# Optimization experiments

Measured on AMD Instinct MI355X. Metric: run time of the kernel, lower is better.

The kernel has to match this reference:

```python
import jax, jax.numpy as jnp
import numpy as np

EMB_DIM = 1024
ATT_DIM = 1024

def setup_inputs() -> dict:
    key = jax.random.key(0)
    ks = jax.random.split(key, 7)
    B, S = 8, 2048
    x_h = jax.random.normal(ks[0], (B, S, EMB_DIM), dtype=jnp.float32)
    # Linear params (stored as [in, out] for x @ W + b)
    sq = 1.0 / np.sqrt(EMB_DIM)
    Wq = jax.random.uniform(ks[1], (EMB_DIM, ATT_DIM), jnp.float32, -sq, sq)
    bq = jax.random.uniform(ks[2], (ATT_DIM,), jnp.float32, -sq, sq)
    Wk = jax.random.uniform(ks[3], (EMB_DIM, ATT_DIM), jnp.float32, -sq, sq)
    bk = jax.random.uniform(ks[4], (ATT_DIM,), jnp.float32, -sq, sq)
    Wv = jax.random.uniform(ks[5], (EMB_DIM, EMB_DIM), jnp.float32, -sq, sq)
    bv = jax.random.uniform(ks[6], (EMB_DIM,), jnp.float32, -sq, sq)
    return {"x_h": x_h, "Wq": Wq, "bq": bq, "Wk": Wk, "bk": bk, "Wv": Wv, "bv": bv}

def reference(x_h, Wq, bq, Wk, bk, Wv, bv):
    q = x_h @ Wq + bq               # [B,S,att_dim]
    k = x_h @ Wk + bk               # [B,S,att_dim]
    v = x_h @ Wv + bv               # [B,S,emb_dim]
    scale = 1.0 / jnp.sqrt(jnp.asarray(k.shape[-1], q.dtype))
    scores = jnp.einsum('bqd,bkd->bqk', q, k) * scale   # [B,S,S]
    # NOTE: original softmaxes over dim=1 (the QUERY axis), not the key axis.
    attn = jax.nn.softmax(scores, axis=1)
    return jnp.einsum('bqk,bkd->bqd', attn, v)
```

## Files before the change

kernel.cpp:

```cpp
#include <hip/hip_runtime.h>
#include <math.h>

typedef __bf16 bf16x8 __attribute__((ext_vector_type(8)));
typedef float f32x4 __attribute__((ext_vector_type(4)));
typedef unsigned short ushort8 __attribute__((ext_vector_type(8)));
typedef unsigned short u16;

#define DEVINL __device__ __forceinline__

DEVINL u16 f2bf(float f) {
    union { float f; unsigned u; } a; a.f = f;
    unsigned u = a.u;
    return (u16)((u + 0x7FFFu + ((u >> 16) & 1u)) >> 16);
}
DEVINL float bf2f(u16 h) { return __uint_as_float(((unsigned)h) << 16); }

DEVINL void gload_lds16(const void* g, void* l) {
    __builtin_amdgcn_global_load_lds(
        (__attribute__((address_space(1))) void*)(g),
        (__attribute__((address_space(3))) void*)(l),
        16, 0, 0);
}

template<int EPI>
__global__ __launch_bounds__(512, 2)
void gemm256(const u16* __restrict__ A, int lda, long sAz,
             const u16* __restrict__ B, int ldb, long sBz,
             void* __restrict__ Cv, int ldc, long sCz,
             const float* __restrict__ bias, float scale, int K)
{
    __shared__ u16 lds[65536];
    const int tid = threadIdx.x;
    const long bz = blockIdx.z;
    const u16* Ab = A + bz * sAz;
    const u16* Bb = B + bz * sBz;
    const int row0 = blockIdx.x * 256, col0 = blockIdx.y * 256;

    const int sr = tid >> 2;
    const int csw = ((tid & 3) * 16) ^ (((sr >> 1) & 3) << 4);
    const u16* Ag = Ab + (long)(row0 + sr) * lda + (csw >> 1);
    const u16* Bg = Bb + (long)(col0 + sr) * ldb + (csw >> 1);
    const int dst0 = tid * 8;

    const int lane = tid & 63, wid = tid >> 6;
    const int wm = wid >> 2, wn = wid & 3;
    const int lane_r = lane & 15;
    const int rdcol = (((lane >> 4) * 16) ^ (((lane_r >> 1) & 3) << 4)) >> 1;
    const int arow0 = wm * 128 + lane_r;
    const int brow0 = wn * 64 + lane_r;

    const int NT = K >> 6;
    f32x4 acc[8][4] = {};
    bf16x8 af[4], bfrag[4];

    auto issueA = [&](int t1, int s, int buf) {
        const u16* g = Ag + (long)t1 * 64 + s * 32;
        u16* d = &lds[(buf * 2 + s) * 8192 + dst0];
        gload_lds16(g, d);
        gload_lds16(g + (long)128 * lda, d + 4096);
    };
    auto issueB = [&](int t1, int s, int buf) {
        const u16* g = Bg + (long)t1 * 64 + s * 32;
        u16* d = &lds[32768 + (buf * 2 + s) * 8192 + dst0];
        gload_lds16(g, d);
        gload_lds16(g + (long)128 * ldb, d + 4096);
    };

#define READ_A(s, h)                                                        \
    _Pragma("unroll")                                                       \
    for (int m = 0; m < 4; ++m)                                             \
        af[m] = *(const bf16x8*)&lds[(buf * 2 + (s)) * 8192 +               \
                     (arow0 + (h) * 64 + m * 16) * 32 + rdcol];

#define READ_B(s)                                                           \
    _Pragma("unroll")                                                       \
    for (int n = 0; n < 4; ++n)                                             \
        bfrag[n] = *(const bf16x8*)&lds[32768 + (buf * 2 + (s)) * 8192 +    \
                     (brow0 + n * 16) * 32 + rdcol];

#define MFMA16(h)                                                           \
    __builtin_amdgcn_s_setprio(1);                                          \
    _Pragma("unroll")                                                       \
    for (int m = 0; m < 4; ++m)                                             \
        _Pragma("unroll")                                                   \
        for (int n = 0; n < 4; ++n)                                         \
            acc[(h) * 4 + m][n] = __builtin_amdgcn_mfma_f32_16x16x32_bf16(  \
                af[m], bfrag[n], acc[(h) * 4 + m][n], 0, 0, 0);             \
    __builtin_amdgcn_s_setprio(0);

    issueA(0, 0, 0); issueB(0, 0, 0); issueA(0, 1, 0); issueB(0, 1, 0);
    asm volatile("s_waitcnt vmcnt(4)" ::: "memory");
    __builtin_amdgcn_s_barrier();

    for (int t = 0; t < NT - 1; ++t) {
        const int buf = t & 1, nbuf = buf ^ 1;
        READ_A(0, 0); READ_B(0);
        issueA(t + 1, 0, nbuf);
        __builtin_amdgcn_s_barrier();
        MFMA16(0);
        __builtin_amdgcn_s_barrier();
        READ_A(0, 1);
        issueB(t + 1, 0, nbuf);
        asm volatile("s_waitcnt vmcnt(4)" ::: "memory");
        __builtin_amdgcn_s_barrier();
        MFMA16(1);
        __builtin_amdgcn_s_barrier();
        READ_A(1, 0); READ_B(1);
        issueA(t + 1, 1, nbuf);
        __builtin_amdgcn_s_barrier();
        MFMA16(0);
        __builtin_amdgcn_s_barrier();
        READ_A(1, 1);
        issueB(t + 1, 1, nbuf);
        asm volatile("s_waitcnt vmcnt(4)" ::: "memory");
        __builtin_amdgcn_s_barrier();
        MFMA16(1);
        __builtin_amdgcn_s_barrier();
    }
    {
        const int buf = (NT - 1) & 1;
        READ_A(0, 0); READ_B(0);
        __builtin_amdgcn_s_barrier();
        MFMA16(0);
        __builtin_amdgcn_s_barrier();
        READ_A(0, 1);
        asm volatile("s_waitcnt vmcnt(0)" ::: "memory");
        __builtin_amdgcn_s_barrier();
        MFMA16(1);
        __builtin_amdgcn_s_barrier();
        READ_A(1, 0); READ_B(1);
        __builtin_amdgcn_s_barrier();
        MFMA16(0);
        __builtin_amdgcn_s_barrier();
        READ_A(1, 1);
        __builtin_amdgcn_s_barrier();
        MFMA16(1);
    }
#undef READ_A
#undef READ_B
#undef MFMA16

    const int crow = (lane >> 4) * 4, ccol = lane & 15;
#pragma unroll
    for (int mf = 0; mf < 8; ++mf)
#pragma unroll
        for (int nf = 0; nf < 4; ++nf) {
            const int gc = col0 + wn * 64 + nf * 16 + ccol;
#pragma unroll
            for (int r = 0; r < 4; ++r) {
                const int gr = row0 + wm * 128 + mf * 16 + crow + r;
                const float v = acc[mf][nf][r];
                if constexpr (EPI == 0) {
                    ((u16*)Cv)[bz * sCz + (long)gr * ldc + gc] = f2bf(v + bias[gc]);
                } else if constexpr (EPI == 1) {
                    ((u16*)Cv)[bz * sCz + (long)gr * ldc + gc] = f2bf(__expf(v * scale));
                } else {
                    ((float*)Cv)[bz * sCz + (long)gr * ldc + gc] = v;
                }
            }
        }
}

__global__ void cast_x_k(const float* __restrict__ x, u16* __restrict__ o)
{
    const int i = blockIdx.x * 256 + threadIdx.x;
    const float4* xv = (const float4*)x;
    const float4 a = xv[(long)i * 2], b = xv[(long)i * 2 + 1];
    ushort8 r;
    r[0] = f2bf(a.x); r[1] = f2bf(a.y); r[2] = f2bf(a.z); r[3] = f2bf(a.w);
    r[4] = f2bf(b.x); r[5] = f2bf(b.y); r[6] = f2bf(b.z); r[7] = f2bf(b.w);
    *(ushort8*)(o + (long)i * 8) = r;
}

__global__ void wt_k(const float* __restrict__ Wq, const float* __restrict__ Wk,
                     const float* __restrict__ Wv, u16* __restrict__ Wt)
{
    __shared__ float t[32][33];
    const int z = blockIdx.z;
    const float* W = (z == 0) ? Wq : ((z == 1) ? Wk : Wv);
    const int k0 = blockIdx.x * 32, n0 = blockIdx.y * 32;
    const int tx = threadIdx.x, ty = threadIdx.y;
#pragma unroll
    for (int j = 0; j < 32; j += 8)
        t[ty + j][tx] = W[(long)(k0 + ty + j) * 1024 + n0 + tx];
    __syncthreads();
#pragma unroll
    for (int j = 0; j < 32; j += 8)
        Wt[((long)z * 1024 + n0 + ty + j) * 1024 + k0 + tx] = f2bf(t[tx][ty + j]);
}

__global__ void bias_k(const float* __restrict__ bq, const float* __restrict__ bk,
                       const float* __restrict__ bv, float* __restrict__ bcat)
{
    const int i = blockIdx.x * 256 + threadIdx.x;
    bcat[i] = (i < 1024) ? bq[i] : ((i < 2048) ? bk[i - 1024] : bv[i - 2048]);
}

__global__ void colsum_k(const u16* __restrict__ E, float* __restrict__ part)
{
    const int b = blockIdx.z, qc = blockIdx.y;
    const int k8 = threadIdx.x;
    const u16* p = E + ((long)b * 2048 + qc * 64) * 2048 + k8 * 8;
    float s[8] = {};
#pragma unroll 4
    for (int q = 0; q < 64; ++q) {
        ushort8 v = *(const ushort8*)(p + (long)q * 2048);
#pragma unroll
        for (int j = 0; j < 8; ++j) s[j] += bf2f(v[j]);
    }
    float* o = part + ((long)b * 32 + qc) * 2048 + k8 * 8;
#pragma unroll
    for (int j = 0; j < 8; ++j) o[j] = s[j];
}

__global__ void rcp_k(const float* __restrict__ part, float* __restrict__ rden)
{
    const int b = blockIdx.y;
    const int k = blockIdx.x * 256 + threadIdx.x;
    float s = 0.f;
#pragma unroll
    for (int qc = 0; qc < 32; ++qc) s += part[((long)b * 32 + qc) * 2048 + k];
    rden[b * 2048 + k] = 1.0f / s;
}

__global__ void vt_k(const u16* __restrict__ qkv, const float* __restrict__ rden,
                     u16* __restrict__ Vt)
{
    __shared__ float t[32][33];
    const int b = blockIdx.z;
    const int k0 = blockIdx.x * 32, d0 = blockIdx.y * 32;
    const int tx = threadIdx.x, ty = threadIdx.y;
#pragma unroll
    for (int j = 0; j < 32; j += 8) {
        const int k = k0 + ty + j;
        t[ty + j][tx] = bf2f(qkv[((long)b * 2048 + k) * 3072 + 2048 + d0 + tx])
                        * rden[b * 2048 + k];
    }
    __syncthreads();
#pragma unroll
    for (int j = 0; j < 32; j += 8)
        Vt[((long)b * 1024 + d0 + ty + j) * 2048 + k0 + tx] = f2bf(t[tx][ty + j]);
}

extern "C" void kernel_launch(void* const* d_in, const int* in_sizes, int n_in,
                              void* d_out, int out_size, void* d_ws, size_t ws_size,
                              hipStream_t stream)
{
    const float* x  = (const float*)d_in[0];
    const float* Wq = (const float*)d_in[1];
    const float* bq = (const float*)d_in[2];
    const float* Wk = (const float*)d_in[3];
    const float* bk = (const float*)d_in[4];
    const float* Wv = (const float*)d_in[5];
    const float* bv = (const float*)d_in[6];

    char* ws = (char*)d_ws;
    u16*   qkv  = (u16*)(ws);
    u16*   E    = (u16*)(ws + 100663296);
    u16*   Vt   = (u16*)(ws + 167772160);
    u16*   xb   = (u16*)(ws + 201326592);
    u16*   Wt   = (u16*)(ws + 234881024);
    float* bcat = (float*)(ws + 241172480);
    float* part = (float*)(ws + 241184768);
    float* rden = (float*)(ws + 243281920);

    const long sQKV = (long)2048 * 3072;
    const long sE   = (long)2048 * 2048;
    const long sVt  = (long)1024 * 2048;
    const long sO   = (long)2048 * 1024;

    cast_x_k<<<8192, 256, 0, stream>>>(x, xb);
    wt_k<<<dim3(32, 32, 3), dim3(32, 8), 0, stream>>>(Wq, Wk, Wv, Wt);
    bias_k<<<12, 256, 0, stream>>>(bq, bk, bv, bcat);
    gemm256<0><<<dim3(64, 12, 1), 512, 0, stream>>>(
        xb, 1024, 0, Wt, 1024, 0, qkv, 3072, 0, bcat, 0.f, 1024);
    gemm256<1><<<dim3(8, 8, 8), 512, 0, stream>>>(
        qkv, 3072, sQKV, qkv + 1024, 3072, sQKV, E, 2048, sE,
        nullptr, 0.03125f, 1024);
    colsum_k<<<dim3(1, 32, 8), 256, 0, stream>>>(E, part);
    rcp_k<<<dim3(8, 8), 256, 0, stream>>>(part, rden);
    vt_k<<<dim3(64, 32, 8), dim3(32, 8), 0, stream>>>(qkv, rden, Vt);
    gemm256<2><<<dim3(8, 4, 8), 512, 0, stream>>>(
        E, 2048, sE, Vt, 2048, sVt, d_out, 1024, sO,
        nullptr, 1.f, 2048);
}
```

Measured before the change: 299.2 us.

## Fuse column-sum into QK^T epilogue, vectorize stores, remap workgroups across XCDs

The QK^T GEMM epilogue now accumulates per-column partial sums of the exponentials and reduces them with cross-lane shuffles into a partial buffer. This removes the separate colsum kernel that re-read the full E matrix. The MFMA operands are swapped so each lane holds four consecutive columns, which allows 4-wide vector stores and vector bias loads in every epilogue. Workgroup IDs are also remapped so that consecutive tiles are spread across the XCDs, aiming for better L2 locality. The cost is extra epilogue shuffles, and a redundant `csum[0] += 0.0f` is left in the code.

```diff
diff --git a/kernel.cpp b/kernel.cpp
--- a/kernel.cpp
+++ b/kernel.cpp
@@ -4,6 +4,7 @@
 typedef __bf16 bf16x8 __attribute__((ext_vector_type(8)));
 typedef float f32x4 __attribute__((ext_vector_type(4)));
 typedef unsigned short ushort8 __attribute__((ext_vector_type(8)));
+typedef unsigned short ushort4v __attribute__((ext_vector_type(4)));
 typedef unsigned short u16;
 
 #define DEVINL __device__ __forceinline__
@@ -27,14 +28,24 @@
 void gemm256(const u16* __restrict__ A, int lda, long sAz,
              const u16* __restrict__ B, int ldb, long sBz,
              void* __restrict__ Cv, int ldc, long sCz,
-             const float* __restrict__ bias, float scale, int K)
+             const float* __restrict__ bias, float* __restrict__ part,
+             float scale, int K)
 {
     __shared__ u16 lds[65536];
     const int tid = threadIdx.x;
-    const long bz = blockIdx.z;
+
+    const int nx = gridDim.x, ny = gridDim.y;
+    const int nwg = nx * ny * gridDim.z;
+    const int orig = blockIdx.x + nx * (blockIdx.y + ny * blockIdx.z);
+    const int id = (orig & 7) * (nwg >> 3) + (orig >> 3);
+    const int tile_x = id % nx;
+    const int rem = id / nx;
+    const int tile_y = rem % ny;
+    const long bz = rem / ny;
+
     const u16* Ab = A + bz * sAz;
     const u16* Bb = B + bz * sBz;
-    const int row0 = blockIdx.x * 256, col0 = blockIdx.y * 256;
+    const int row0 = tile_x * 256, col0 = tile_y * 256;
 
     const int sr = tid >> 2;
     const int csw = ((tid & 3) * 16) ^ (((sr >> 1) & 3) << 4);
@@ -85,7 +96,7 @@
         _Pragma("unroll")                                                   \
         for (int n = 0; n < 4; ++n)                                         \
             acc[(h) * 4 + m][n] = __builtin_amdgcn_mfma_f32_16x16x32_bf16(  \
-                af[m], bfrag[n], acc[(h) * 4 + m][n], 0, 0, 0);             \
+                bfrag[n], af[m], acc[(h) * 4 + m][n], 0, 0, 0);             \
     __builtin_amdgcn_s_setprio(0);
 
     issueA(0, 0, 0); issueB(0, 0, 0); issueA(0, 1, 0); issueB(0, 1, 0);
@@ -140,25 +151,62 @@
 #undef READ_B
 #undef MFMA16
 
-    const int crow = (lane >> 4) * 4, ccol = lane & 15;
-#pragma unroll
-    for (int mf = 0; mf < 8; ++mf)
+    const int erow = lane & 15, ecol0 = (lane >> 4) * 4;
+    float4 bias4[4];
+    if constexpr (EPI == 0) {
+#pragma unroll
+        for (int nf = 0; nf < 4; ++nf)
+            bias4[nf] = *(const float4*)&bias[col0 + wn * 64 + nf * 16 + ecol0];
+    }
+    f32x4 csum[4] = {};
+#pragma unroll
+    for (int mf = 0; mf < 8; ++mf) {
+        const int gr = row0 + wm * 128 + mf * 16 + erow;
 #pragma unroll
         for (int nf = 0; nf < 4; ++nf) {
-            const int gc = col0 + wn * 64 + nf * 16 + ccol;
-#pragma unroll
-            for (int r = 0; r < 4; ++r) {
-                const int gr = row0 + wm * 128 + mf * 16 + crow + r;
-                const float v = acc[mf][nf][r];
-                if constexpr (EPI == 0) {
-                    ((u16*)Cv)[bz * sCz + (long)gr * ldc + gc] = f2bf(v + bias[gc]);
-                } else if constexpr (EPI == 1) {
-                    ((u16*)Cv)[bz * sCz + (long)gr * ldc + gc] = f2bf(__expf(v * scale));
-                } else {
-                    ((float*)Cv)[bz * sCz + (long)gr * ldc + gc] = v;
-                }
+            const int gc = col0 + wn * 64 + nf * 16 + ecol0;
+            f32x4 v = acc[mf][nf];
+            if constexpr (EPI == 0) {
+                v[0] += bias4[nf].x; v[1] += bias4[nf].y;
+                v[2] += bias4[nf].z; v[3] += bias4[nf].w;
+                ushort4v o = { f2bf(v[0]), f2bf(v[1]), f2bf(v[2]), f2bf(v[3]) };
+                *(ushort4v*)((u16*)Cv + bz * sCz + (long)gr * ldc + gc) = o;
+            } else if constexpr (EPI == 1) {
+                f32x4 e;
+#pragma unroll
+                for (int r = 0; r < 4; ++r) e[r] = __expf(v[r] * scale);
+                csum[0] += 0.0f;
+                csum[nf] += e;
+                ushort4v o = { f2bf(e[0]), f2bf(e[1]), f2bf(e[2]), f2bf(e[3]) };
+                *(ushort4v*)((u16*)Cv + bz * sCz + (long)gr * ldc + gc) = o;
+            } else {
+                *(float4*)((float*)Cv + bz * sCz + (long)gr * ldc + gc) =
+                    make_float4(v[0], v[1], v[2], v[3]);
             }
         }
+    }
+    if constexpr (EPI == 1) {
+#pragma unroll
+        for (int nf = 0; nf < 4; ++nf)
+#pragma unroll
+            for (int r = 0; r < 4; ++r) {
+                float s = csum[nf][r];
+                s += __shfl_xor(s, 1);
+                s += __shfl_xor(s, 2);
+                s += __shfl_xor(s, 4);
+                s += __shfl_xor(s, 8);
+                csum[nf][r] = s;
+            }
+        if ((lane & 15) == 0) {
+#pragma unroll
+            for (int nf = 0; nf < 4; ++nf) {
+                float* p = part + ((bz * 16 + (long)tile_x * 2 + wm) * 2048)
+                         + col0 + wn * 64 + nf * 16 + ecol0;
+                *(float4*)p = make_float4(csum[nf][0], csum[nf][1],
+                                          csum[nf][2], csum[nf][3]);
+            }
+        }
+    }
 }
 
 __global__ void cast_x_k(const float* __restrict__ x, u16* __restrict__ o)
@@ -196,30 +244,13 @@
     bcat[i] = (i < 1024) ? bq[i] : ((i < 2048) ? bk[i - 1024] : bv[i - 2048]);
 }
 
-__global__ void colsum_k(const u16* __restrict__ E, float* __restrict__ part)
-{
-    const int b = blockIdx.z, qc = blockIdx.y;
-    const int k8 = threadIdx.x;
-    const u16* p = E + ((long)b * 2048 + qc * 64) * 2048 + k8 * 8;
-    float s[8] = {};
-#pragma unroll 4
-    for (int q = 0; q < 64; ++q) {
-        ushort8 v = *(const ushort8*)(p + (long)q * 2048);
-#pragma unroll
-        for (int j = 0; j < 8; ++j) s[j] += bf2f(v[j]);
-    }
-    float* o = part + ((long)b * 32 + qc) * 2048 + k8 * 8;
-#pragma unroll
-    for (int j = 0; j < 8; ++j) o[j] = s[j];
-}
-
 __global__ void rcp_k(const float* __restrict__ part, float* __restrict__ rden)
 {
     const int b = blockIdx.y;
     const int k = blockIdx.x * 256 + threadIdx.x;
     float s = 0.f;
 #pragma unroll
-    for (int qc = 0; qc < 32; ++qc) s += part[((long)b * 32 + qc) * 2048 + k];
+    for (int c = 0; c < 16; ++c) s += part[((long)b * 16 + c) * 2048 + k];
     rden[b * 2048 + k] = 1.0f / s;
 }
 
@@ -273,14 +304,13 @@
     wt_k<<<dim3(32, 32, 3), dim3(32, 8), 0, stream>>>(Wq, Wk, Wv, Wt);
     bias_k<<<12, 256, 0, stream>>>(bq, bk, bv, bcat);
     gemm256<0><<<dim3(64, 12, 1), 512, 0, stream>>>(
-        xb, 1024, 0, Wt, 1024, 0, qkv, 3072, 0, bcat, 0.f, 1024);
+        xb, 1024, 0, Wt, 1024, 0, qkv, 3072, 0, bcat, nullptr, 0.f, 1024);
     gemm256<1><<<dim3(8, 8, 8), 512, 0, stream>>>(
         qkv, 3072, sQKV, qkv + 1024, 3072, sQKV, E, 2048, sE,
-        nullptr, 0.03125f, 1024);
-    colsum_k<<<dim3(1, 32, 8), 256, 0, stream>>>(E, part);
+        nullptr, part, 0.03125f, 1024);
     rcp_k<<<dim3(8, 8), 256, 0, stream>>>(part, rden);
     vt_k<<<dim3(64, 32, 8), dim3(32, 8), 0, stream>>>(qkv, rden, Vt);
     gemm256<2><<<dim3(8, 4, 8), 512, 0, stream>>>(
         E, 2048, sE, Vt, 2048, sVt, d_out, 1024, sO,
-        nullptr, 1.f, 2048);
-}
+        nullptr, nullptr, 1.f, 2048);
+}
```

Measured after the change: 304.4 us. No clear change (+1.7%).
